# Kernel tuning notes

Hardware: AMD Instinct MI355X
Metric: run time of the kernel (lower is better)

## Reference

```python
import jax, jax.numpy as jnp
import numpy as np

N, C, T, H, W = 16, 64, 30, 64, 44
PC = 64
OUT_H, OUT_W = 16, 20
T_RATE, H_RATE, W_RATE = 0.4, 4.0 / 8, 10.0 / 11  # torso
HEAD_H_RATE = 1.0 / 8
EPS = 1e-8


def setup_inputs() -> dict:
    key = jax.random.key(0)
    ks = jax.random.split(key, 8)
    x = jax.random.normal(ks[0], (N, C, T, H, W), jnp.float32)
    param_x = jax.random.normal(ks[1], (N, PC), jnp.float32)
    W1 = jax.random.normal(ks[2], (PC, PC // 2), jnp.float32) * 0.1
    b1 = jnp.zeros((PC // 2,), jnp.float32)
    W2 = jax.random.normal(ks[3], (PC // 2, 7), jnp.float32) * 0.1
    b2 = jnp.zeros((7,), jnp.float32)
    Wf = jax.random.normal(ks[4], (C, C), jnp.float32) * 0.05
    bf = jnp.zeros((C,), jnp.float32)
    return {"x": x, "param_x": param_x, "W1": W1, "b1": b1, "W2": W2, "b2": b2, "Wf": Wf, "bf": bf}


def reference(x, param_x, W1, b1, W2, b2, Wf, bf):
    n, c, t, h, w = x.shape
    dtype = x.dtype
    atten_in_t = t * T_RATE
    atten_in_h = h * H_RATE
    atten_in_w = w * W_RATE
    atten_ratio = atten_in_w / atten_in_h
    aout_h = int(round(OUT_W / atten_ratio))
    anchor_t = int(round(t / 2.0))
    anchor_x = int(round(w / 2.0))
    anchor_y = int(round(atten_in_h / 2.0 + h * HEAD_H_RATE))  # torso anchor

    # --- localization MLP (locator stand-in): param_x -> 7 params per sample ---
    hid = jnp.tanh(param_x @ W1 + b1)
    p = hid @ W2 + b2  # [N, 7]
    dt0, dx0, dy0 = p[:, 0:1], p[:, 1:2], p[:, 2:3]
    log_sigma2, log_delta_t, log_delta, log_gamma = p[:, 3:4], p[:, 4:5], p[:, 5:6], p[:, 6:7]

    dx = jnp.tanh(dx0) * atten_in_w / 2.0 + anchor_x          # [N,1]
    dy = jnp.tanh(dy0) * atten_in_h / 2.0 + anchor_y          # [N,1]
    sigma2 = jnp.exp(log_sigma2)                              # [N,1]
    delta = jnp.exp(log_delta) * W_RATE                      # [N,1]
    gamma = jax.nn.sigmoid(log_gamma)                         # [N,1]

    # --- spatial Gaussian filter banks ---
    gx = jnp.arange(OUT_W, dtype=dtype)
    gy = jnp.arange(aout_h, dtype=dtype)
    mu_x = dx + (gx - OUT_W / 2.0) * delta                    # [N, OUT_W]
    mu_y = dy + (gy - aout_h / 2.0) * delta                   # [N, aout_h]
    a = jnp.arange(w, dtype=dtype)
    b = jnp.arange(h, dtype=dtype)
    s2 = sigma2[:, :, None]                                   # [N,1,1]
    Fx = jnp.exp(-((a - mu_x[:, :, None]) ** 2) / (2.0 * s2))  # [N, OUT_W, W]
    Fy = jnp.exp(-((b - mu_y[:, :, None]) ** 2) / (2.0 * s2))  # [N, aout_h, H]
    Fx = Fx / jnp.maximum(jnp.sum(Fx, -1, keepdims=True), EPS)
    Fy = Fy / jnp.maximum(jnp.sum(Fy, -1, keepdims=True), EPS)

    # --- spatial sampling: Fy @ x @ Fx^T over the (C*T)-folded batch dim ---
    x2 = x.reshape(n, c * t, h, w)
    t1 = jnp.einsum('ndhw,nqw->ndhq', x2, Fx)                 # [N, C*T, H, OUT_W]
    g = jnp.einsum('nph,ndhq->ndpq', Fy, t1)                  # [N, C*T, aout_h, OUT_W]
    pad_t = (OUT_H - aout_h) // 2
    pad_b = OUT_H - pad_t - aout_h
    g = jnp.pad(g, ((0, 0), (0, 0), (pad_t, pad_b), (0, 0)))  # [N, C*T, OUT_H, OUT_W]

    # --- temporal linear resampling (grid_sample, align_corners=True, zero pad) ---
    dt = jnp.tanh(dt0) * atten_in_t / 2.0 + anchor_t          # [N,1]
    delta_t = jnp.exp(log_delta_t) * T_RATE                   # [N,1]
    gt = jnp.arange(t, dtype=dtype)
    mu_t = dt + (gt - t / 2.0) * delta_t                      # [N, T] raw frame positions

    gseq = g.reshape(n, c, t, OUT_H * OUT_W).transpose(0, 1, 3, 2).reshape(n, c * OUT_H * OUT_W, t)
    i0f = jnp.floor(mu_t)
    frac = mu_t - i0f
    i0 = i0f.astype(jnp.int32)
    i1 = i0 + 1

    def gather(idx):
        return jnp.take_along_axis(gseq, jnp.clip(idx, 0, t - 1)[:, None, :], axis=2)

    w0 = jnp.where((i0 >= 0) & (i0 < t), 1.0 - frac, 0.0)[:, None, :]
    w1 = jnp.where((i1 >= 0) & (i1 < t), frac, 0.0)[:, None, :]
    samp = gather(i0) * w0 + gather(i1) * w1                  # [N, C*OUT_H*OUT_W, T]
    out = samp.reshape(n, c, OUT_H, OUT_W, t).transpose(0, 1, 4, 2, 3)  # [N,C,T,OUT_H,OUT_W]

    out = out * gamma.reshape(n, 1, 1, 1, 1)
    # feature extraction: pointwise Conv3d (extractor stand-in)
    out = jnp.einsum('ncthw,oc->nothw', out, Wf) + bf[None, :, None, None, None]

    params = jnp.stack([dt[:, 0], dx[:, 0], dy[:, 0], sigma2[:, 0],
                        delta[:, 0], delta_t[:, 0], gamma[:, 0]], 0)  # [7, N]
    return out, jax.lax.stop_gradient(params)
```

## Files before the change

kernel.cpp:

```cpp
#include <hip/hip_runtime.h>
#include <math.h>

#define NN 16
#define CC 64
#define TT 30
#define HH 64
#define WW 44
#define OUTH 16
#define OUTW 20
#define HW 320

#define FXT_OFF   0
#define FY_OFF    14080
#define IDX0_OFF  30464
#define IDX1_OFF  30944
#define TW0_OFF   31424
#define TW1_OFF   31904
#define GAM_OFF   32384
#define RNG_OFF   32400
#define G_OFF     32464

__global__ __launch_bounds__(64) void params_kernel(
    const float* __restrict__ param_x, const float* __restrict__ W1,
    const float* __restrict__ b1, const float* __restrict__ W2,
    const float* __restrict__ b2, float* __restrict__ ws,
    float* __restrict__ params_out) {
  int n = blockIdx.x;
  int tid = threadIdx.x;
  __shared__ float px[64];
  __shared__ float hid[32];
  __shared__ float pv[7];

  px[tid] = param_x[n * 64 + tid];
  __syncthreads();
  if (tid < 32) {
    float s = b1[tid];
    #pragma unroll
    for (int k = 0; k < 64; ++k) s += px[k] * W1[k * 32 + tid];
    hid[tid] = tanhf(s);
  }
  __syncthreads();
  if (tid < 7) {
    float s = b2[tid];
    #pragma unroll
    for (int j = 0; j < 32; ++j) s += hid[j] * W2[j * 7 + tid];
    pv[tid] = s;
  }
  __syncthreads();

  float dt      = tanhf(pv[0]) * 6.0f  + 15.0f;
  float dx      = tanhf(pv[1]) * 20.0f + 22.0f;
  float dy      = tanhf(pv[2]) * 16.0f + 24.0f;
  float sigma2  = expf(pv[3]);
  float delta_t = expf(pv[4]) * 0.4f;
  float delta   = expf(pv[5]) * (10.0f / 11.0f);
  float gamma   = 1.0f / (1.0f + expf(-pv[6]));
  float inv2s2  = 1.0f / (2.0f * sigma2);

  if (tid < 20) {
    float mu = dx + ((float)tid - 10.0f) * delta;
    float vals[44];
    float s = 0.0f;
    #pragma unroll
    for (int w = 0; w < 44; ++w) {
      float d = (float)w - mu;
      float e = expf(-d * d * inv2s2);
      vals[w] = e; s += e;
    }
    float inv = 1.0f / fmaxf(s, 1e-8f);
    float* FxT = ws + FXT_OFF + n * (44 * 20) + tid;
    #pragma unroll
    for (int w = 0; w < 44; ++w) FxT[w * 20] = vals[w] * inv;
  }
  if (tid < 16) {
    float mu = dy + ((float)tid - 8.0f) * delta;
    float vals[64];
    float s = 0.0f;
    #pragma unroll
    for (int h = 0; h < 64; ++h) {
      float d = (float)h - mu;
      float e = expf(-d * d * inv2s2);
      vals[h] = e; s += e;
    }
    float inv = 1.0f / fmaxf(s, 1e-8f);
    float* Fy = ws + FY_OFF + n * (16 * 64) + tid * 64;
    #pragma unroll
    for (int h = 0; h < 64; ++h) Fy[h] = vals[h] * inv;
  }
  if (tid < 30) {
    float mu = dt + ((float)tid - 15.0f) * delta_t;
    float i0f = floorf(mu);
    float frac = mu - i0f;
    int i0 = (int)i0f;
    int i1 = i0 + 1;
    float w0 = (i0 >= 0 && i0 < TT) ? (1.0f - frac) : 0.0f;
    float w1 = (i1 >= 0 && i1 < TT) ? frac : 0.0f;
    ((int*)(ws + IDX0_OFF))[n * TT + tid] = min(max(i0, 0), TT - 1);
    ((int*)(ws + IDX1_OFF))[n * TT + tid] = min(max(i1, 0), TT - 1);
    ws[TW0_OFF + n * TT + tid] = w0;
    ws[TW1_OFF + n * TT + tid] = w1;
  }
  if (tid == 0) {
    float R = 7.7459667f * sqrtf(sigma2);
    int wlo = max(0,  (int)floorf(dx - 10.0f * delta - R));
    int whi = min(43, (int)ceilf (dx +  9.0f * delta + R));
    int hlo = max(0,  (int)floorf(dy -  8.0f * delta - R));
    int hhi = min(63, (int)ceilf (dy +  7.0f * delta + R));
    int* rng = (int*)(ws + RNG_OFF) + n * 4;
    rng[0] = wlo & ~3;
    rng[1] = whi | 3;
    rng[2] = hlo & ~3;
    rng[3] = hhi | 3;

    ws[GAM_OFF + n] = gamma;
    params_out[0 * NN + n] = dt;
    params_out[1 * NN + n] = dx;
    params_out[2 * NN + n] = dy;
    params_out[3 * NN + n] = sigma2;
    params_out[4 * NN + n] = delta;
    params_out[5 * NN + n] = delta_t;
    params_out[6 * NN + n] = gamma;
  }
}

__global__ __launch_bounds__(256) void spatial_kernel(
    const float* __restrict__ x, const float* __restrict__ ws,
    float* __restrict__ g) {
  int b = blockIdx.x;
  int n  = b / (TT * 16);
  int r  = b % (TT * 16);
  int t  = r / 16;
  int c0 = (r % 16) * 4;

  int tid  = threadIdx.x;
  int cl   = tid >> 6;
  int lane = tid & 63;

  __shared__ float st1[4 * 20 * 68];
  __shared__ float sFy[16 * 68];

  const int* rng = (const int*)(ws + RNG_OFF) + n * 4;
  int wlo4 = __builtin_amdgcn_readfirstlane(rng[0]);
  int whi4 = __builtin_amdgcn_readfirstlane(rng[1]);
  int hlo4 = __builtin_amdgcn_readfirstlane(rng[2]);
  int hhi4 = __builtin_amdgcn_readfirstlane(rng[3]);

  {
    const float4* Fy4 = (const float4*)(ws + FY_OFF + n * (16 * 64));
    float4 v = Fy4[tid];
    int p = tid >> 4, h4 = tid & 15;
    *(float4*)&sFy[p * 68 + h4 * 4] = v;
  }

  int c = c0 + cl;
  bool hact = (lane >= hlo4) && (lane <= hhi4);
  const float4* xp =
      (const float4*)(x + ((((size_t)n * CC + c) * TT + t) * HH + lane) * WW);
  const float* fxt = ws + FXT_OFF + n * (44 * 20);

  float acc[20];
  #pragma unroll
  for (int q = 0; q < 20; ++q) acc[q] = 0.0f;

  int ilo = wlo4 >> 2, ihi = whi4 >> 2;
  for (int i = ilo; i <= ihi; ++i) {
    float4 v = make_float4(0.0f, 0.0f, 0.0f, 0.0f);
    if (hact) v = xp[i];
    float vx[4] = {v.x, v.y, v.z, v.w};
    const float* fr = fxt + i * 80;
    #pragma unroll
    for (int k = 0; k < 4; ++k) {
      #pragma unroll
      for (int q = 0; q < 20; ++q)
        acc[q] = fmaf(vx[k], fr[k * 20 + q], acc[q]);
    }
  }
  if (hact) {
    #pragma unroll
    for (int q = 0; q < 20; ++q) st1[(cl * 20 + q) * 68 + lane] = acc[q];
  }
  __syncthreads();

  int hh = lane >> 5;
  int pp = (lane >> 2) & 7;
  int qg = lane & 3;
  int hc0 = hlo4 >> 2, hc1 = hhi4 >> 2;

  float o[2][5];
  #pragma unroll
  for (int u = 0; u < 2; ++u)
    #pragma unroll
    for (int j = 0; j < 5; ++j) o[u][j] = 0.0f;

  for (int hcc = hc0 + hh; hcc <= hc1; hcc += 2) {
    float4 fy0 = *(const float4*)&sFy[pp * 68 + hcc * 4];
    float4 fy1 = *(const float4*)&sFy[(pp + 8) * 68 + hcc * 4];
    #pragma unroll
    for (int j = 0; j < 5; ++j) {
      int q = qg * 5 + j;
      float4 tv = *(const float4*)&st1[(cl * 20 + q) * 68 + hcc * 4];
      o[0][j] = fmaf(fy0.x, tv.x,
                fmaf(fy0.y, tv.y, fmaf(fy0.z, tv.z, fmaf(fy0.w, tv.w, o[0][j]))));
      o[1][j] = fmaf(fy1.x, tv.x,
                fmaf(fy1.y, tv.y, fmaf(fy1.z, tv.z, fmaf(fy1.w, tv.w, o[1][j]))));
    }
  }
  #pragma unroll
  for (int u = 0; u < 2; ++u)
    #pragma unroll
    for (int j = 0; j < 5; ++j)
      o[u][j] += __shfl_xor(o[u][j], 32);

  if (hh == 0) {
    float* gout = g + ((size_t)((n * CC + c) * TT + t)) * HW;
    #pragma unroll
    for (int u = 0; u < 2; ++u) {
      int p = pp + u * 8;
      #pragma unroll
      for (int j = 0; j < 5; ++j) gout[p * OUTW + qg * 5 + j] = o[u][j];
    }
  }
}

__global__ __launch_bounds__(256) void output_kernel(
    const float* __restrict__ g, const float* __restrict__ ws,
    const float* __restrict__ Wf, const float* __restrict__ bf,
    float* __restrict__ out) {
  int b = blockIdx.x;
  int n    = b / (TT * 2);
  int r    = b % (TT * 2);
  int tp   = r >> 1;
  int hw0  = (r & 1) * 160;
  int tid  = threadIdx.x;

  __shared__ float sWfT[64 * 65];
  __shared__ float smix[64 * 160];

  #pragma unroll
  for (int i = tid; i < 64 * 64; i += 256) {
    int oc = i >> 6, c = i & 63;
    sWfT[c * 65 + oc] = Wf[i];
  }

  int i0 = ((const int*)(ws + IDX0_OFF))[n * TT + tp];
  int i1 = ((const int*)(ws + IDX1_OFF))[n * TT + tp];
  float w0 = ws[TW0_OFF + n * TT + tp];
  float w1 = ws[TW1_OFF + n * TT + tp];
  float gamma = ws[GAM_OFF + n];

  #pragma unroll
  for (int i4 = tid; i4 < 64 * 40; i4 += 256) {
    int c  = i4 / 40;
    int r4 = i4 - c * 40;
    size_t base = (size_t)(n * CC + c) * TT;
    float4 a  = *(const float4*)(g + (base + i0) * HW + hw0 + r4 * 4);
    float4 bb = *(const float4*)(g + (base + i1) * HW + hw0 + r4 * 4);
    float4 m;
    m.x = gamma * fmaf(w0, a.x, w1 * bb.x);
    m.y = gamma * fmaf(w0, a.y, w1 * bb.y);
    m.z = gamma * fmaf(w0, a.z, w1 * bb.z);
    m.w = gamma * fmaf(w0, a.w, w1 * bb.w);
    *(float4*)&smix[c * 160 + r4 * 4] = m;
  }
  __syncthreads();

  int ocg = tid >> 5;
  int hwg = tid & 31;
  int oc0 = ocg * 8;
  int hwl0 = hwg * 5;
  float acc[8][5];
  #pragma unroll
  for (int u = 0; u < 8; ++u)
    #pragma unroll
    for (int j = 0; j < 5; ++j) acc[u][j] = 0.0f;

  #pragma unroll 4
  for (int c = 0; c < 64; ++c) {
    float4 wv0 = *(const float4*)&sWfT[c * 65 + oc0];
    float4 wv1 = *(const float4*)&sWfT[c * 65 + oc0 + 4];
    float m[5];
    #pragma unroll
    for (int j = 0; j < 5; ++j) m[j] = smix[c * 160 + hwl0 + j];
    float wv[8] = {wv0.x, wv0.y, wv0.z, wv0.w, wv1.x, wv1.y, wv1.z, wv1.w};
    #pragma unroll
    for (int u = 0; u < 8; ++u)
      #pragma unroll
      for (int j = 0; j < 5; ++j) acc[u][j] = fmaf(wv[u], m[j], acc[u][j]);
  }

  #pragma unroll
  for (int u = 0; u < 8; ++u) {
    int oc = oc0 + u;
    float bias = bf[oc];
    float* op = out + (((size_t)n * CC + oc) * TT + tp) * HW + hw0 + hwl0;
    #pragma unroll
    for (int j = 0; j < 5; ++j) op[j] = acc[u][j] + bias;
  }
}

extern "C" void kernel_launch(void* const* d_in, const int* in_sizes, int n_in,
                              void* d_out, int out_size, void* d_ws,
                              size_t ws_size, hipStream_t stream) {
  const float* x       = (const float*)d_in[0];
  const float* param_x = (const float*)d_in[1];
  const float* W1      = (const float*)d_in[2];
  const float* b1      = (const float*)d_in[3];
  const float* W2      = (const float*)d_in[4];
  const float* b2      = (const float*)d_in[5];
  const float* Wf      = (const float*)d_in[6];
  const float* bf      = (const float*)d_in[7];
  float* out = (float*)d_out;
  float* ws  = (float*)d_ws;
  float* params_out = out + (size_t)NN * CC * TT * HW;

  params_kernel<<<NN, 64, 0, stream>>>(param_x, W1, b1, W2, b2, ws, params_out);
  spatial_kernel<<<NN * TT * 16, 256, 0, stream>>>(x, ws, ws + G_OFF);
  output_kernel<<<NN * TT * 2, 256, 0, stream>>>(ws + G_OFF, ws, Wf, bf, out);
}
```

Baseline: 523.6 us.

## Skip spatial filtering for frames outside sampled temporal range; preload x row

The params kernel computes the minimum and maximum clamped temporal indices used by the interpolation and stores them with the spatial ranges. The spatial kernel exits early for frames that are never gathered, removing their loads and FMAs. The x row loads are also unrolled into a register array so all loads issue before the FMA loop. Risks are higher register pressure and leaving g uninitialized for skipped frames, which must never be read.

```diff
diff --git a/kernel.cpp b/kernel.cpp
--- a/kernel.cpp
+++ b/kernel.cpp
@@ -18,7 +18,7 @@
 #define TW1_OFF   31904
 #define GAM_OFF   32384
 #define RNG_OFF   32400
-#define G_OFF     32464
+#define G_OFF     32512
 
 __global__ __launch_bounds__(64) void params_kernel(
     const float* __restrict__ param_x, const float* __restrict__ W1,
@@ -30,8 +30,10 @@
   __shared__ float px[64];
   __shared__ float hid[32];
   __shared__ float pv[7];
+  __shared__ int tmin_s, tmax_s;
 
   px[tid] = param_x[n * 64 + tid];
+  if (tid == 0) { tmin_s = TT; tmax_s = -1; }
   __syncthreads();
   if (tid < 32) {
     float s = b1[tid];
@@ -95,22 +97,29 @@
     int i1 = i0 + 1;
     float w0 = (i0 >= 0 && i0 < TT) ? (1.0f - frac) : 0.0f;
     float w1 = (i1 >= 0 && i1 < TT) ? frac : 0.0f;
-    ((int*)(ws + IDX0_OFF))[n * TT + tid] = min(max(i0, 0), TT - 1);
-    ((int*)(ws + IDX1_OFF))[n * TT + tid] = min(max(i1, 0), TT - 1);
+    int i0c = min(max(i0, 0), TT - 1);
+    int i1c = min(max(i1, 0), TT - 1);
+    ((int*)(ws + IDX0_OFF))[n * TT + tid] = i0c;
+    ((int*)(ws + IDX1_OFF))[n * TT + tid] = i1c;
     ws[TW0_OFF + n * TT + tid] = w0;
     ws[TW1_OFF + n * TT + tid] = w1;
-  }
+    atomicMin(&tmin_s, i0c);
+    atomicMax(&tmax_s, i1c);
+  }
+  __syncthreads();
   if (tid == 0) {
     float R = 7.7459667f * sqrtf(sigma2);
     int wlo = max(0,  (int)floorf(dx - 10.0f * delta - R));
     int whi = min(43, (int)ceilf (dx +  9.0f * delta + R));
     int hlo = max(0,  (int)floorf(dy -  8.0f * delta - R));
     int hhi = min(63, (int)ceilf (dy +  7.0f * delta + R));
-    int* rng = (int*)(ws + RNG_OFF) + n * 4;
+    int* rng = (int*)(ws + RNG_OFF) + n * 6;
     rng[0] = wlo & ~3;
     rng[1] = whi | 3;
     rng[2] = hlo & ~3;
     rng[3] = hhi | 3;
+    rng[4] = tmin_s;
+    rng[5] = tmax_s;
 
     ws[GAM_OFF + n] = gamma;
     params_out[0 * NN + n] = dt;
@@ -139,11 +148,15 @@
   __shared__ float st1[4 * 20 * 68];
   __shared__ float sFy[16 * 68];
 
-  const int* rng = (const int*)(ws + RNG_OFF) + n * 4;
+  const int* rng = (const int*)(ws + RNG_OFF) + n * 6;
   int wlo4 = __builtin_amdgcn_readfirstlane(rng[0]);
   int whi4 = __builtin_amdgcn_readfirstlane(rng[1]);
   int hlo4 = __builtin_amdgcn_readfirstlane(rng[2]);
   int hhi4 = __builtin_amdgcn_readfirstlane(rng[3]);
+  int tlo  = __builtin_amdgcn_readfirstlane(rng[4]);
+  int thi  = __builtin_amdgcn_readfirstlane(rng[5]);
+
+  if (t < tlo || t > thi) return;
 
   {
     const float4* Fy4 = (const float4*)(ws + FY_OFF + n * (16 * 64));
@@ -156,23 +169,35 @@
   bool hact = (lane >= hlo4) && (lane <= hhi4);
   const float4* xp =
       (const float4*)(x + ((((size_t)n * CC + c) * TT + t) * HH + lane) * WW);
+  int ilo = wlo4 >> 2, ihi = whi4 >> 2;
+
+  float xrow[44];
+  #pragma unroll
+  for (int i = 0; i < 11; ++i) {
+    float4 v = make_float4(0.0f, 0.0f, 0.0f, 0.0f);
+    if (i >= ilo && i <= ihi) {
+      if (hact) v = xp[i];
+    }
+    xrow[4 * i + 0] = v.x; xrow[4 * i + 1] = v.y;
+    xrow[4 * i + 2] = v.z; xrow[4 * i + 3] = v.w;
+  }
+
   const float* fxt = ws + FXT_OFF + n * (44 * 20);
-
   float acc[20];
   #pragma unroll
   for (int q = 0; q < 20; ++q) acc[q] = 0.0f;
 
-  int ilo = wlo4 >> 2, ihi = whi4 >> 2;
-  for (int i = ilo; i <= ihi; ++i) {
-    float4 v = make_float4(0.0f, 0.0f, 0.0f, 0.0f);
-    if (hact) v = xp[i];
-    float vx[4] = {v.x, v.y, v.z, v.w};
-    const float* fr = fxt + i * 80;
-    #pragma unroll
-    for (int k = 0; k < 4; ++k) {
+  #pragma unroll
+  for (int i = 0; i < 11; ++i) {
+    if (i >= ilo && i <= ihi) {
+      const float* fr = fxt + i * 80;
       #pragma unroll
-      for (int q = 0; q < 20; ++q)
-        acc[q] = fmaf(vx[k], fr[k * 20 + q], acc[q]);
+      for (int k = 0; k < 4; ++k) {
+        float xv = xrow[4 * i + k];
+        #pragma unroll
+        for (int q = 0; q < 20; ++q)
+          acc[q] = fmaf(xv, fr[k * 20 + q], acc[q]);
+      }
     }
   }
   if (hact) {
```

Measured after the change: 476.5 us. 1.1x faster.
